# Performance work log

Hardware: AMD Instinct MI355X
Metric: run time of the kernel (lower is better)

## Reference

```python
import jax, jax.numpy as jnp
import numpy as np

D_STATE = 16
DT_RANK = 48
D_CONV = 4
EPS = 1e-5


def rmsnorm(x, w):
    return x * jax.lax.rsqrt(jnp.mean(x * x, axis=-1, keepdims=True) + EPS) * w


def causal_dw_conv(u, w, b):
    # u: [B,T,D], w: [D,K] depthwise causal kernel, b: [D]
    B, T, D = u.shape
    K = w.shape[1]
    up = jnp.pad(u, ((0, 0), (K - 1, 0), (0, 0)))
    acc = jnp.zeros_like(u)
    for k in range(K):  # K=4, tiny fixed loop
        acc = acc + up[:, k:k + T, :] * w[:, k]
    return acc + b


def mamba_mixer(h, ipw, cw, cb, xpw, dpw, dpb, alog, dpar, opw):
    # h: [B,T,d_model]
    B, T, _ = h.shape
    xz = h @ ipw.T                       # [B,T,2*d_inner]
    u, z = jnp.split(xz, 2, axis=-1)     # each [B,T,d_inner]
    u = jax.nn.silu(causal_dw_conv(u, cw, cb))
    xp = u @ xpw.T                       # [B,T,dt_rank+2*d_state]
    dt = xp[..., :DT_RANK]
    Bm = xp[..., DT_RANK:DT_RANK + D_STATE]
    Cm = xp[..., DT_RANK + D_STATE:]
    delta = jax.nn.softplus(dt @ dpw.T + dpb)      # [B,T,d_inner]
    A = -jnp.exp(alog)                              # [d_inner, d_state], negative
    dA = jnp.exp(delta[..., None] * A)              # [B,T,d_inner,d_state] in (0,1)
    dBu = (delta * u)[..., None] * Bm[:, :, None, :]
    # time-major for scan
    dA_t = jnp.moveaxis(dA, 1, 0)
    dBu_t = jnp.moveaxis(dBu, 1, 0)
    C_t = jnp.moveaxis(Cm, 1, 0)

    def step(hst, inp):
        a, bu, c = inp
        hst = a * hst + bu                          # [B,d_inner,d_state]
        y = jnp.einsum('bdn,bn->bd', hst, c)
        return hst, y

    h0 = jnp.zeros((B, u.shape[-1], D_STATE), u.dtype)
    _, ys = jax.lax.scan(step, h0, (dA_t, dBu_t, C_t))
    y = jnp.moveaxis(ys, 0, 1) + u * dpar           # skip via D
    y = y * jax.nn.silu(z)                          # gate
    return y @ opw.T                                # [B,T,d_model]


def setup_inputs() -> dict:
    key = jax.random.key(0)
    ks = jax.random.split(key, 16)
    L, d_model, d_inner = 4, 768, 1536
    B, C, T = 4, 256, 512
    s = 0.02
    return {
        'x': jax.random.normal(ks[0], (B, C, T), jnp.float32),
        'in_proj_w': jax.random.normal(ks[1], (L, 2 * d_inner, d_model), jnp.float32) * s,
        'conv_w': jax.random.normal(ks[2], (L, d_inner, D_CONV), jnp.float32) * 0.3,
        'conv_b': jnp.zeros((L, d_inner), jnp.float32),
        'x_proj_w': jax.random.normal(ks[3], (L, DT_RANK + 2 * D_STATE, d_inner), jnp.float32) * s,
        'dt_proj_w': jax.random.normal(ks[4], (L, d_inner, DT_RANK), jnp.float32) * 0.1,
        'dt_proj_b': jax.random.normal(ks[5], (L, d_inner), jnp.float32) * 0.1 - 4.0,
        'A_log': jax.random.uniform(ks[6], (L, d_inner, D_STATE), jnp.float32, 0.0, 1.5),
        'D_param': jax.random.uniform(ks[7], (L, d_inner), jnp.float32),
        'out_proj_w': jax.random.normal(ks[8], (L, d_model, d_inner), jnp.float32) * s,
        'norm_w': jnp.ones((L, d_model), jnp.float32),
        'norm_f_w': jnp.ones((d_model,), jnp.float32),
        'inp_w': jax.random.normal(ks[9], (d_model, C), jnp.float32) * s,
        'inp_b': jnp.zeros((d_model,), jnp.float32),
        'cls_w': jax.random.normal(ks[10], (10, d_model), jnp.float32) * s,
        'cls_b': jnp.zeros((10,), jnp.float32),
    }


def reference(x, in_proj_w, conv_w, conv_b, x_proj_w, dt_proj_w, dt_proj_b,
              A_log, D_param, out_proj_w, norm_w, norm_f_w,
              inp_w, inp_b, cls_w, cls_b):
    # x: (B, C, T) -> (B, T, C)
    xt = jnp.transpose(x, (0, 2, 1))
    h = xt @ inp_w.T + inp_b                # [B,T,d_model]
    hidden = h
    residual = None
    L = in_proj_w.shape[0]
    for l in range(L):
        residual = hidden if residual is None else hidden + residual
        normed = rmsnorm(residual, norm_w[l])
        hidden = mamba_mixer(normed, in_proj_w[l], conv_w[l], conv_b[l],
                             x_proj_w[l], dt_proj_w[l], dt_proj_b[l],
                             A_log[l], D_param[l], out_proj_w[l])
    residual = hidden + residual
    hidden = rmsnorm(residual, norm_f_w)
    pooled = hidden.mean(axis=1)            # [B,d_model]
    logits = pooled @ cls_w.T + cls_b       # [B,num_labels]
    return logits
```

## Files before the change

### kernel.cpp

```cpp
#include <hip/hip_runtime.h>
#include <math.h>

#define D_MODEL 768
#define D_INNER 1536
#define B_SZ 4
#define T_SZ 512
#define ROWS (B_SZ*T_SZ)
#define XP_N 80
#define CH 16
#define CT 32
#define XS 8
#define XKC (D_INNER/XS)
#define OS 4
#define OKC (D_INNER/OS)
#define MN_OUT (ROWS*768)

typedef __attribute__((ext_vector_type(8))) short bf16x8;
typedef __attribute__((ext_vector_type(4))) float f32x4;

#define GLL(g, l) __builtin_amdgcn_global_load_lds( \
    (const __attribute__((address_space(1))) void*)(g), \
    (__attribute__((address_space(3))) void*)(l), 16, 0, 0)

__device__ __forceinline__ float sigmoidf_(float x){ return 1.0f/(1.0f+__expf(-x)); }
__device__ __forceinline__ float siluf_(float x){ return x*sigmoidf_(x); }
__device__ __forceinline__ unsigned short f2bf(float f){
  unsigned u = __builtin_bit_cast(unsigned, f);
  u = (u + 0x7FFFu + ((u >> 16) & 1u)) >> 16;
  return (unsigned short)u;
}

__global__ __launch_bounds__(256) void gemm_bf16(
    const unsigned short* __restrict__ A, const unsigned short* __restrict__ Wb,
    float* __restrict__ C, int M, int N, int K)
{
  __shared__ unsigned short As[128*32];
  __shared__ unsigned short Ws[128*32];
  const int tid = threadIdx.x;
  const int bm = blockIdx.y*128, bn = blockIdx.x*128;
  const int wave = tid >> 6, lane = tid & 63;
  const int wm = (wave >> 1)*64, wn = (wave & 1)*64;
  const int fr = lane & 15, quad = lane >> 4;
  f32x4 acc[4][4] = {};
  const int row0 = (wave*64 + lane) >> 2;
  const int khp  = lane & 3;
  const int khl  = (khp + 4 - ((row0 >> 1) & 3)) & 3;
  const unsigned short* Ag = A  + (size_t)(bm + row0)*K + khl*8;
  const unsigned short* Wg = Wb + (size_t)(bn + row0)*K + khl*8;
  const size_t rstep = (size_t)64*K;
  unsigned short* ldsA = As + wave*512;
  unsigned short* ldsW = Ws + wave*512;

  for (int k0 = 0; k0 < K; k0 += 32){
    GLL(Ag + k0,          ldsA);
    GLL(Ag + rstep + k0,  ldsA + 2048);
    GLL(Wg + k0,          ldsW);
    GLL(Wg + rstep + k0,  ldsW + 2048);
    __syncthreads();
    bf16x8 a[4], b[4];
    #pragma unroll
    for (int i=0;i<4;i++){
      const int row = wm + i*16 + fr;
      a[i] = *(const bf16x8*)(As + row*32 + (((quad + (row>>1)) & 3)*8));
    }
    #pragma unroll
    for (int j=0;j<4;j++){
      const int row = wn + j*16 + fr;
      b[j] = *(const bf16x8*)(Ws + row*32 + (((quad + (row>>1)) & 3)*8));
    }
    #pragma unroll
    for (int i=0;i<4;i++)
      #pragma unroll
      for (int j=0;j<4;j++)
        acc[i][j] = __builtin_amdgcn_mfma_f32_16x16x32_bf16(a[i], b[j], acc[i][j], 0, 0, 0);
    __syncthreads();
  }
  #pragma unroll
  for (int i=0;i<4;i++){
    #pragma unroll
    for (int r=0;r<4;r++){
      const int row = bm + wm + i*16 + quad*4 + r;
      float* Cp = C + (size_t)row*N + bn + wn + fr;
      #pragma unroll
      for (int j=0;j<4;j++)
        Cp[j*16] = acc[i][j][r];
    }
  }
}

__global__ __launch_bounds__(256) void gemm_bf16_sk(
    const unsigned short* __restrict__ A, const unsigned short* __restrict__ Wb,
    float* __restrict__ P0, float* __restrict__ P1, int M, int N, int K)
{
  __shared__ unsigned short As[128*32];
  __shared__ unsigned short Ws[128*32];
  const int tid = threadIdx.x;
  const int bm = blockIdx.y*128, bn = blockIdx.x*128;
  const int s = blockIdx.z;
  const int koff = s*OKC;
  const int wave = tid >> 6, lane = tid & 63;
  const int wm = (wave >> 1)*64, wn = (wave & 1)*64;
  const int fr = lane & 15, quad = lane >> 4;
  f32x4 acc[4][4] = {};
  const int row0 = (wave*64 + lane) >> 2;
  const int khp  = lane & 3;
  const int khl  = (khp + 4 - ((row0 >> 1) & 3)) & 3;
  const unsigned short* Ag = A  + (size_t)(bm + row0)*K + koff + khl*8;
  const unsigned short* Wg = Wb + (size_t)(bn + row0)*K + koff + khl*8;
  const size_t rstep = (size_t)64*K;
  unsigned short* ldsA = As + wave*512;
  unsigned short* ldsW = Ws + wave*512;

  for (int k0 = 0; k0 < OKC; k0 += 32){
    GLL(Ag + k0,          ldsA);
    GLL(Ag + rstep + k0,  ldsA + 2048);
    GLL(Wg + k0,          ldsW);
    GLL(Wg + rstep + k0,  ldsW + 2048);
    __syncthreads();
    bf16x8 a[4], b[4];
    #pragma unroll
    for (int i=0;i<4;i++){
      const int row = wm + i*16 + fr;
      a[i] = *(const bf16x8*)(As + row*32 + (((quad + (row>>1)) & 3)*8));
    }
    #pragma unroll
    for (int j=0;j<4;j++){
      const int row = wn + j*16 + fr;
      b[j] = *(const bf16x8*)(Ws + row*32 + (((quad + (row>>1)) & 3)*8));
    }
    #pragma unroll
    for (int i=0;i<4;i++)
      #pragma unroll
      for (int j=0;j<4;j++)
        acc[i][j] = __builtin_amdgcn_mfma_f32_16x16x32_bf16(a[i], b[j], acc[i][j], 0, 0, 0);
    __syncthreads();
  }
  float* Cb = (s < 2 ? P0 : P1) + (size_t)(s & 1)*MN_OUT;
  #pragma unroll
  for (int i=0;i<4;i++){
    #pragma unroll
    for (int r=0;r<4;r++){
      const int row = bm + wm + i*16 + quad*4 + r;
      float* Cp = Cb + (size_t)row*N + bn + wn + fr;
      #pragma unroll
      for (int j=0;j<4;j++)
        Cp[j*16] = acc[i][j][r];
    }
  }
}

__global__ __launch_bounds__(256) void sgemm_input(
    const float* __restrict__ x, const float* __restrict__ W,
    const float* __restrict__ bias, float* __restrict__ C)
{
  __shared__ float As[16][64];
  __shared__ float Wsh[16][64];
  const int bm = blockIdx.y*64, bn = blockIdx.x*64;
  const int b = bm >> 9, t0 = bm & (T_SZ-1);
  const int tid = threadIdx.x;
  const int tx = tid & 15, ty = tid >> 4;
  const int lm = tid & 63, lk = (tid >> 6) << 2;
  float acc[4][4] = {};
  const float* Wp = W + (size_t)(bn+lm)*256 + lk;
  const float* xb = x + ((size_t)b*256)*512 + t0 + lm;
  for (int k0 = 0; k0 < 256; k0 += 16){
    #pragma unroll
    for (int i=0;i<4;i++)
      As[lk+i][lm] = xb[(size_t)(k0+lk+i)*512];
    float4 wv = *(const float4*)(Wp + k0);
    Wsh[lk+0][lm]=wv.x; Wsh[lk+1][lm]=wv.y; Wsh[lk+2][lm]=wv.z; Wsh[lk+3][lm]=wv.w;
    __syncthreads();
    #pragma unroll
    for (int k = 0; k < 16; k++){
      float a[4], w[4];
      #pragma unroll
      for (int i=0;i<4;i++) a[i] = As[k][ty*4+i];
      #pragma unroll
      for (int j=0;j<4;j++) w[j] = Wsh[k][tx*4+j];
      #pragma unroll
      for (int i=0;i<4;i++)
        #pragma unroll
        for (int j=0;j<4;j++)
          acc[i][j] += a[i]*w[j];
    }
    __syncthreads();
  }
  #pragma unroll
  for (int i=0;i<4;i++){
    const int r = bm + ty*4 + i;
    #pragma unroll
    for (int j=0;j<4;j++){
      const int n = bn + tx*4 + j;
      C[(size_t)r*768 + n] = acc[i][j] + bias[n];
    }
  }
}

__global__ __launch_bounds__(256) void xproj_conv_splitk(
    const float* __restrict__ xz, const float* __restrict__ cw,
    const float* __restrict__ cb, const float* __restrict__ W,
    float* __restrict__ part)
{
  __shared__ float As[16][64];
  __shared__ float Wsh[16][80];
  const int bm = blockIdx.x*64;
  const int s = blockIdx.y;
  const int koff = s*XKC;
  const int tid = threadIdx.x;
  const int tx = tid & 15, ty = tid >> 4;
  const int lm = tid & 63, lk = (tid >> 6) << 2;
  float acc[4][5] = {};
  const int row = bm + lm;
  const int t = row & (T_SZ-1);
  for (int k0 = 0; k0 < XKC; k0 += 16){
    const int d0 = koff + k0 + lk;
    float4 cbv = *(const float4*)(cb + d0);
    float cba[4] = {cbv.x, cbv.y, cbv.z, cbv.w};
    float4 tp3 = *(const float4*)(xz + (size_t)row*3072 + d0);
    float4 tp0 = (t>=3) ? *(const float4*)(xz + (size_t)(row-3)*3072 + d0) : make_float4(0.f,0.f,0.f,0.f);
    float4 tp1 = (t>=2) ? *(const float4*)(xz + (size_t)(row-2)*3072 + d0) : make_float4(0.f,0.f,0.f,0.f);
    float4 tp2 = (t>=1) ? *(const float4*)(xz + (size_t)(row-1)*3072 + d0) : make_float4(0.f,0.f,0.f,0.f);
    float a0[4]={tp0.x,tp0.y,tp0.z,tp0.w}, a1[4]={tp1.x,tp1.y,tp1.z,tp1.w};
    float a2[4]={tp2.x,tp2.y,tp2.z,tp2.w}, a3[4]={tp3.x,tp3.y,tp3.z,tp3.w};
    #pragma unroll
    for (int i=0;i<4;i++){
      const float4 w4 = *(const float4*)(cw + (size_t)(d0+i)*4);
      float a = cba[i];
      a += a0[i]*w4.x; a += a1[i]*w4.y; a += a2[i]*w4.z; a += a3[i]*w4.w;
      As[lk+i][lm] = siluf_(a);
    }
    for (int i = tid; i < 320; i += 256){
      const int wr = i % 80, wk = (i / 80) << 2;
      float4 wv = *(const float4*)(W + (size_t)wr*D_INNER + koff + k0 + wk);
      Wsh[wk+0][wr]=wv.x; Wsh[wk+1][wr]=wv.y; Wsh[wk+2][wr]=wv.z; Wsh[wk+3][wr]=wv.w;
    }
    __syncthreads();
    #pragma unroll
    for (int k = 0; k < 16; k++){
      float a[4], w[5];
      #pragma unroll
      for (int i=0;i<4;i++) a[i] = As[k][ty*4+i];
      #pragma unroll
      for (int j=0;j<5;j++) w[j] = Wsh[k][tx*5+j];
      #pragma unroll
      for (int i=0;i<4;i++)
        #pragma unroll
        for (int j=0;j<5;j++)
          acc[i][j] += a[i]*w[j];
    }
    __syncthreads();
  }
  #pragma unroll
  for (int i=0;i<4;i++){
    const int r = bm + ty*4 + i;
    #pragma unroll
    for (int j=0;j<5;j++){
      const int n = tx*5 + j;
      part[((size_t)s*ROWS + r)*XP_N + n] = acc[i][j];
    }
  }
}

__global__ __launch_bounds__(256) void dtproj_fused(
    const float* __restrict__ part, const float* __restrict__ W,
    const float* __restrict__ bias, float* __restrict__ delta,
    float* __restrict__ xpbc)
{
  if (blockIdx.x >= 24){
    const int i = ((blockIdx.x - 24)*32 + blockIdx.y)*256 + threadIdx.x;
    const int r = i >> 5, cc = i & 31;
    float ssum = 0.f;
    #pragma unroll
    for (int s2=0;s2<XS;s2++)
      ssum += part[((size_t)s2*ROWS + r)*XP_N + 48 + cc];
    xpbc[(size_t)r*32 + cc] = ssum;
    return;
  }
  __shared__ float As[16][64];
  __shared__ float Wsh[16][64];
  const int bm = blockIdx.y*64, bn = blockIdx.x*64;
  const int tid = threadIdx.x;
  const int tx = tid & 15, ty = tid >> 4;
  const int lm = tid & 63, lk = (tid >> 6) << 2;
  float acc[4][4] = {};
  const float* Ap = part + (size_t)(bm+lm)*XP_N + lk;
  const float* Wp = W + (size_t)(bn+lm)*48 + lk;
  for (int k0 = 0; k0 < 48; k0 += 16){
    float4 av = make_float4(0.f,0.f,0.f,0.f);
    #pragma unroll
    for (int s2=0;s2<XS;s2++){
      const float4 pv = *(const float4*)(Ap + (size_t)s2*ROWS*XP_N + k0);
      av.x += pv.x; av.y += pv.y; av.z += pv.z; av.w += pv.w;
    }
    float4 wv = *(const float4*)(Wp + k0);
    As[lk+0][lm]=av.x; As[lk+1][lm]=av.y; As[lk+2][lm]=av.z; As[lk+3][lm]=av.w;
    Wsh[lk+0][lm]=wv.x; Wsh[lk+1][lm]=wv.y; Wsh[lk+2][lm]=wv.z; Wsh[lk+3][lm]=wv.w;
    __syncthreads();
    #pragma unroll
    for (int k = 0; k < 16; k++){
      float a[4], w[4];
      #pragma unroll
      for (int i=0;i<4;i++) a[i] = As[k][ty*4+i];
      #pragma unroll
      for (int j=0;j<4;j++) w[j] = Wsh[k][tx*4+j];
      #pragma unroll
      for (int i=0;i<4;i++)
        #pragma unroll
        for (int j=0;j<4;j++)
          acc[i][j] += a[i]*w[j];
    }
    __syncthreads();
  }
  #pragma unroll
  for (int i=0;i<4;i++){
    const int r = bm + ty*4 + i;
    #pragma unroll
    for (int j=0;j<4;j++){
      const int n = bn + tx*4 + j;
      float v = acc[i][j] + bias[n];
      v = (v > 20.f) ? v : log1pf(__expf(v));
      delta[(size_t)r*D_INNER + n] = v;
    }
  }
}

__global__ __launch_bounds__(256) void scan_pass1(
    const float* __restrict__ delta, const float* __restrict__ xz,
    const float* __restrict__ xpbc, const float* __restrict__ alog,
    const float* __restrict__ cw, const float* __restrict__ cb,
    float* __restrict__ Pend, float* __restrict__ Hend)
{
  const int d = blockIdx.x*256 + threadIdx.x;
  const int b = blockIdx.y, c = blockIdx.z;
  float4 t0 = *(const float4*)(alog + d*16 + 0);
  float4 t1 = *(const float4*)(alog + d*16 + 4);
  float4 t2 = *(const float4*)(alog + d*16 + 8);
  float4 t3 = *(const float4*)(alog + d*16 + 12);
  float Av[16] = {t0.x,t0.y,t0.z,t0.w,t1.x,t1.y,t1.z,t1.w,
                  t2.x,t2.y,t2.z,t2.w,t3.x,t3.y,t3.z,t3.w};
  float h[16], P[16];
  #pragma unroll
  for (int n=0;n<16;n++){ Av[n] = -__expf(Av[n]); h[n]=0.f; P[n]=1.f; }
  const size_t row0 = (size_t)b*T_SZ + (size_t)c*CT;
  const float* dp  = delta + row0*D_INNER + d;
  const float* xp0 = xz    + row0*3072 + d;
  const float* bp  = xpbc  + row0*32;
  const float4 cwv = *(const float4*)(cw + (size_t)d*4);
  const float cbv = cb[d];
  float xm3, xm2, xm1;
  if (c == 0){ xm3 = xm2 = xm1 = 0.f; }
  else { xm3 = xp0[-3*3072]; xm2 = xp0[-2*3072]; xm1 = xp0[-1*3072]; }
  #pragma unroll 4
  for (int tt=0; tt<CT; tt++){
    const float dv = dp[(size_t)tt*D_INNER];
    const float xc = xp0[(size_t)tt*3072];
    float ua = cbv;
    ua += xm3*cwv.x; ua += xm2*cwv.y; ua += xm1*cwv.z; ua += xc*cwv.w;
    const float uv = siluf_(ua);
    xm3 = xm2; xm2 = xm1; xm1 = xc;
    const float4 B0 = *(const float4*)(bp + (size_t)tt*32);
    const float4 B1 = *(const float4*)(bp + (size_t)tt*32 + 4);
    const float4 B2 = *(const float4*)(bp + (size_t)tt*32 + 8);
    const float4 B3 = *(const float4*)(bp + (size_t)tt*32 + 12);
    const float Bv[16] = {B0.x,B0.y,B0.z,B0.w,B1.x,B1.y,B1.z,B1.w,
                          B2.x,B2.y,B2.z,B2.w,B3.x,B3.y,B3.z,B3.w};
    const float du = dv*uv;
    #pragma unroll
    for (int n=0;n<16;n++){
      const float dA = __expf(dv*Av[n]);
      P[n] *= dA;
      h[n] = dA*h[n] + du*Bv[n];
    }
  }
  float* Pp = Pend + ((size_t)(b*CH+c)*D_INNER + d)*16;
  float* Hp = Hend + ((size_t)(b*CH+c)*D_INNER + d)*16;
  *(float4*)(Pp+ 0) = make_float4(P[0],P[1],P[2],P[3]);
  *(float4*)(Pp+ 4) = make_float4(P[4],P[5],P[6],P[7]);
  *(float4*)(Pp+ 8) = make_float4(P[8],P[9],P[10],P[11]);
  *(float4*)(Pp+12) = make_float4(P[12],P[13],P[14],P[15]);
  *(float4*)(Hp+ 0) = make_float4(h[0],h[1],h[2],h[3]);
  *(float4*)(Hp+ 4) = make_float4(h[4],h[5],h[6],h[7]);
  *(float4*)(Hp+ 8) = make_float4(h[8],h[9],h[10],h[11]);
  *(float4*)(Hp+12) = make_float4(h[12],h[13],h[14],h[15]);
}

__global__ __launch_bounds__(256) void scan_combine(
    const float* __restrict__ Pend, const float* __restrict__ Hend,
    float* __restrict__ Hin)
{
  const int gid = blockIdx.x*256 + threadIdx.x;
  const int b = gid / (D_INNER*16);
  const int r = gid % (D_INNER*16);
  const size_t base = (size_t)b*CH*D_INNER*16 + r;
  const size_t step = (size_t)D_INNER*16;
  float h = 0.f;
  Hin[base] = 0.f;
  #pragma unroll
  for (int c=0; c<CH-1; c++){
    h = Pend[base + (size_t)c*step]*h + Hend[base + (size_t)c*step];
    Hin[base + (size_t)(c+1)*step] = h;
  }
}

__global__ __launch_bounds__(256) void scan_pass3(
    const float* __restrict__ delta, const float* __restrict__ xz,
    const float* __restrict__ xpbc, const float* __restrict__ alog,
    const float* __restrict__ cw, const float* __restrict__ cb,
    const float* __restrict__ Dp, const float* __restrict__ Hin,
    unsigned short* __restrict__ yb)
{
  const int d = blockIdx.x*256 + threadIdx.x;
  const int b = blockIdx.y, c = blockIdx.z;
  float4 t0 = *(const float4*)(alog + d*16 + 0);
  float4 t1 = *(const float4*)(alog + d*16 + 4);
  float4 t2 = *(const float4*)(alog + d*16 + 8);
  float4 t3 = *(const float4*)(alog + d*16 + 12);
  float Av[16] = {t0.x,t0.y,t0.z,t0.w,t1.x,t1.y,t1.z,t1.w,
                  t2.x,t2.y,t2.z,t2.w,t3.x,t3.y,t3.z,t3.w};
  #pragma unroll
  for (int n=0;n<16;n++) Av[n] = -__expf(Av[n]);
  const float* Hp = Hin + ((size_t)(b*CH+c)*D_INNER + d)*16;
  float4 h0 = *(const float4*)(Hp+0);
  float4 h1 = *(const float4*)(Hp+4);
  float4 h2 = *(const float4*)(Hp+8);
  float4 h3 = *(const float4*)(Hp+12);
  float h[16] = {h0.x,h0.y,h0.z,h0.w,h1.x,h1.y,h1.z,h1.w,
                 h2.x,h2.y,h2.z,h2.w,h3.x,h3.y,h3.z,h3.w};
  const float Dv = Dp[d];
  const size_t row0 = (size_t)b*T_SZ + (size_t)c*CT;
  const float* dp  = delta + row0*D_INNER + d;
  const float* xp0 = xz    + row0*3072 + d;
  const float* zp  = xz    + row0*3072 + 1536 + d;
  const float* bp  = xpbc  + row0*32;
  unsigned short* yp = yb + row0*D_INNER + d;
  const float4 cwv = *(const float4*)(cw + (size_t)d*4);
  const float cbv = cb[d];
  float xm3, xm2, xm1;
  if (c == 0){ xm3 = xm2 = xm1 = 0.f; }
  else { xm3 = xp0[-3*3072]; xm2 = xp0[-2*3072]; xm1 = xp0[-1*3072]; }
  #pragma unroll 2
  for (int tt=0; tt<CT; tt++){
    const float dv = dp[(size_t)tt*D_INNER];
    const float xc = xp0[(size_t)tt*3072];
    const float zv = zp[(size_t)tt*3072];
    float ua = cbv;
    ua += xm3*cwv.x; ua += xm2*cwv.y; ua += xm1*cwv.z; ua += xc*cwv.w;
    const float uv = siluf_(ua);
    xm3 = xm2; xm2 = xm1; xm1 = xc;
    const float4 B0 = *(const float4*)(bp + (size_t)tt*32);
    const float4 B1 = *(const float4*)(bp + (size_t)tt*32 + 4);
    const float4 B2 = *(const float4*)(bp + (size_t)tt*32 + 8);
    const float4 B3 = *(const float4*)(bp + (size_t)tt*32 + 12);
    const float4 C0 = *(const float4*)(bp + (size_t)tt*32 + 16);
    const float4 C1 = *(const float4*)(bp + (size_t)tt*32 + 20);
    const float4 C2 = *(const float4*)(bp + (size_t)tt*32 + 24);
    const float4 C3 = *(const float4*)(bp + (size_t)tt*32 + 28);
    const float Bv[16] = {B0.x,B0.y,B0.z,B0.w,B1.x,B1.y,B1.z,B1.w,
                          B2.x,B2.y,B2.z,B2.w,B3.x,B3.y,B3.z,B3.w};
    const float Cv[16] = {C0.x,C0.y,C0.z,C0.w,C1.x,C1.y,C1.z,C1.w,
                          C2.x,C2.y,C2.z,C2.w,C3.x,C3.y,C3.z,C3.w};
    const float du = dv*uv;
    float p = 0.f;
    #pragma unroll
    for (int n=0;n<16;n++){
      const float dA = __expf(dv*Av[n]);
      h[n] = dA*h[n] + du*Bv[n];
      p += h[n]*Cv[n];
    }
    yp[(size_t)tt*D_INNER] = f2bf((p + uv*Dv)*siluf_(zv));
  }
}

__global__ __launch_bounds__(256) void fused_norm_cast(
    float* __restrict__ resid, const float* __restrict__ P0, const float* __restrict__ P1,
    const float* __restrict__ w, unsigned short* __restrict__ obf, float* __restrict__ ofp,
    const float* __restrict__ cin1, unsigned short* __restrict__ co1, int cn1, int cnb1,
    const float* __restrict__ cin2, unsigned short* __restrict__ co2, int cn2)
{
  const int blk = blockIdx.x;
  if (blk >= 2048){
    const int cb = blk - 2048;
    const float* in; unsigned short* o; int i4;
    if (cb < cnb1){ in = cin1; o = co1; i4 = (cb*256 + threadIdx.x)*4; if (i4 >= cn1) return; }
    else { in = cin2; o = co2; i4 = ((cb-cnb1)*256 + threadIdx.x)*4; if (i4 >= cn2) return; }
    float4 v = *(const float4*)(in + i4);
    ushort4 r;
    r.x = f2bf(v.x); r.y = f2bf(v.y); r.z = f2bf(v.z); r.w = f2bf(v.w);
    *(ushort4*)(o + i4) = r;
    return;
  }
  const int row = blk;
  const int tid = threadIdx.x;
  float v[3];
  float ss = 0.f;
  #pragma unroll
  for (int i=0;i<3;i++){
    const int c = tid + i*256;
    const size_t idx = (size_t)row*768 + c;
    float r = resid[idx];
    if (P0) r += (P0[idx] + P0[MN_OUT + idx]) + (P1[idx] + P1[MN_OUT + idx]);
    v[i] = r;
    ss += r*r;
  }
  #pragma unroll
  for (int off=32; off>=1; off>>=1) ss += __shfl_xor(ss, off);
  __shared__ float sred[4];
  const int lane = tid & 63, wv = tid >> 6;
  if (lane == 0) sred[wv] = ss;
  __syncthreads();
  const float tot = sred[0]+sred[1]+sred[2]+sred[3];
  const float scale = rsqrtf(tot*(1.0f/768.0f) + 1e-5f);
  #pragma unroll
  for (int i=0;i<3;i++){
    const int c = tid + i*256;
    const size_t idx = (size_t)row*768 + c;
    if (P0) resid[idx] = v[i];
    const float o = v[i]*scale*w[c];
    if (obf) obf[idx] = f2bf(o);
    else     ofp[idx] = o;
  }
}

__global__ __launch_bounds__(256) void pool_partial(const float* __restrict__ normed,
                                                    float* __restrict__ part){
  const int i = blockIdx.x*256 + threadIdx.x;
  const int s = blockIdx.y;
  const int b = i / 768, m = i % 768;
  float sum = 0.f;
  const float* p = normed + ((size_t)b*T_SZ + s*32)*768 + m;
  #pragma unroll
  for (int t=0; t<32; t++) sum += p[(size_t)t*768];
  part[s*3072 + i] = sum;
}

__global__ __launch_bounds__(256) void pool_cls(const float* __restrict__ part,
                                                const float* __restrict__ cw,
                                                const float* __restrict__ cb,
                                                float* __restrict__ out){
  __shared__ float ls[768];
  const int b = blockIdx.x;
  const int tid = threadIdx.x;
  #pragma unroll
  for (int i=0;i<3;i++){
    const int m = tid + i*256;
    float s = 0.f;
    #pragma unroll
    for (int c=0;c<16;c++) s += part[c*3072 + b*768 + m];
    ls[m] = s * (1.0f/T_SZ);
  }
  __syncthreads();
  const int wave = tid >> 6, lane = tid & 63;
  for (int o = wave; o < 10; o += 4){
    float s = 0.f;
    for (int k = lane; k < 768; k += 64) s += ls[k]*cw[o*768 + k];
    #pragma unroll
    for (int off=32; off>=1; off>>=1) s += __shfl_xor(s, off);
    if (lane == 0) out[b*10 + o] = s + cb[o];
  }
}

extern "C" void kernel_launch(void* const* d_in, const int* in_sizes, int n_in,
                              void* d_out, int out_size, void* d_ws, size_t ws_size,
                              hipStream_t stream) {
  const float* x         = (const float*)d_in[0];
  const float* in_proj_w = (const float*)d_in[1];
  const float* conv_w    = (const float*)d_in[2];
  const float* conv_b    = (const float*)d_in[3];
  const float* x_proj_w  = (const float*)d_in[4];
  const float* dt_proj_w = (const float*)d_in[5];
  const float* dt_proj_b = (const float*)d_in[6];
  const float* A_log     = (const float*)d_in[7];
  const float* D_param   = (const float*)d_in[8];
  const float* out_proj_w= (const float*)d_in[9];
  const float* norm_w    = (const float*)d_in[10];
  const float* norm_f_w  = (const float*)d_in[11];
  const float* inp_w     = (const float*)d_in[12];
  const float* inp_b     = (const float*)d_in[13];
  const float* cls_w     = (const float*)d_in[14];
  const float* cls_b     = (const float*)d_in[15];
  float* out = (float*)d_out;

  char* ws = (char*)d_ws;
  auto carve = [&](size_t nelem)->float* {
    float* p = (float*)ws;
    ws += ((nelem*sizeof(float) + 255)/256)*256;
    return p;
  };
  float* resid  = carve((size_t)ROWS*768);
  float* normed = carve((size_t)ROWS*768);
  float* hidden = carve((size_t)ROWS*768);
  float* xz     = carve((size_t)ROWS*3072);
  float* ucv    = carve((size_t)ROWS*1536);
  float* xpbc   = carve((size_t)ROWS*32);
  float* delta  = carve((size_t)ROWS*1536);
  float* ybf_f  = carve((size_t)ROWS*1536/2);
  float* wbi_f  = carve((size_t)(3072*768)/2);
  float* wbo_f  = carve((size_t)(768*1536)/2);
  float* Hin    = carve((size_t)B_SZ*CH*D_INNER*16);
  float* xpart  = carve((size_t)XS*ROWS*XP_N);
  float* ppool  = carve((size_t)16*3072);

  unsigned short* normedb = (unsigned short*)normed;
  unsigned short* ybf = (unsigned short*)ybf_f;
  unsigned short* wbi = (unsigned short*)wbi_f;
  unsigned short* wbo = (unsigned short*)wbo_f;
  float* Pend = normed;
  float* Hend = hidden;

  sgemm_input<<<dim3(12,32), 256, 0, stream>>>(x, inp_w, inp_b, resid);

  for (int l = 0; l < 4; l++){
    fused_norm_cast<<<2048 + 2304 + 1152, 256, 0, stream>>>(
        resid, l ? delta : nullptr, l ? ucv : nullptr,
        norm_w + (size_t)l*768, normedb, nullptr,
        in_proj_w + (size_t)l*3072*768, wbi, 3072*768, 2304,
        out_proj_w + (size_t)l*768*1536, wbo, 768*1536);
    gemm_bf16<<<dim3(24,16), 256, 0, stream>>>(normedb, wbi, xz, ROWS, 3072, 768);
    xproj_conv_splitk<<<dim3(32,XS), 256, 0, stream>>>(
        xz, conv_w + (size_t)l*1536*4, conv_b + (size_t)l*1536,
        x_proj_w + (size_t)l*XP_N*1536, xpart);
    dtproj_fused<<<dim3(32,32), 256, 0, stream>>>(
        xpart, dt_proj_w + (size_t)l*1536*48, dt_proj_b + (size_t)l*1536, delta, xpbc);
    scan_pass1<<<dim3(6,B_SZ,CH-1), 256, 0, stream>>>(
        delta, xz, xpbc, A_log + (size_t)l*1536*16,
        conv_w + (size_t)l*1536*4, conv_b + (size_t)l*1536, Pend, Hend);
    scan_combine<<<(B_SZ*D_INNER*16)/256, 256, 0, stream>>>(Pend, Hend, Hin);
    scan_pass3<<<dim3(6,B_SZ,CH), 256, 0, stream>>>(
        delta, xz, xpbc, A_log + (size_t)l*1536*16,
        conv_w + (size_t)l*1536*4, conv_b + (size_t)l*1536,
        D_param + (size_t)l*1536, Hin, ybf);
    gemm_bf16_sk<<<dim3(6,16,OS), 256, 0, stream>>>(ybf, wbo, delta, ucv, ROWS, 768, 1536);
  }

  fused_norm_cast<<<2048, 256, 0, stream>>>(
      resid, delta, ucv, norm_f_w, nullptr, normed,
      nullptr, nullptr, 0, 0, nullptr, nullptr, 0);
  pool_partial<<<dim3(12,16), 256, 0, stream>>>(normed, ppool);
  pool_cls<<<4, 256, 0, stream>>>(ppool, cls_w, cls_b, out);
}
```

Baseline: 842.8 us.

## Shrink GEMM M-tile to 64, double scan chunks, compute chunk decay via delta sum

Both bf16 GEMMs now use 64x128 tiles, with each wave owning a 64x32 slab, which doubles the grid to get more blocks onto the CUs. The selective scan moves from 16 chunks of 32 steps to 32 chunks of 16 steps for more parallelism. The per-chunk decay product is now taken as exp(A*sum(delta)) rather than a running product, dropping a multiply per state per step. Pend and Hend get their own workspace buffers because the larger chunk count no longer fits in the aliased normed/hidden buffers; the trade-off is lower MFMA reuse per block and more combine work.

```diff
diff --git a/kernel.cpp b/kernel.cpp
--- a/kernel.cpp
+++ b/kernel.cpp
@@ -7,8 +7,8 @@
 #define T_SZ 512
 #define ROWS (B_SZ*T_SZ)
 #define XP_N 80
-#define CH 16
-#define CT 32
+#define CH 32
+#define CT 16
 #define XS 8
 #define XKC (D_INNER/XS)
 #define OS 4
@@ -34,16 +34,17 @@
     const unsigned short* __restrict__ A, const unsigned short* __restrict__ Wb,
     float* __restrict__ C, int M, int N, int K)
 {
-  __shared__ unsigned short As[128*32];
+  __shared__ unsigned short As[64*32];
   __shared__ unsigned short Ws[128*32];
   const int tid = threadIdx.x;
-  const int bm = blockIdx.y*128, bn = blockIdx.x*128;
+  const int bm = blockIdx.y*64, bn = blockIdx.x*128;
   const int wave = tid >> 6, lane = tid & 63;
-  const int wm = (wave >> 1)*64, wn = (wave & 1)*64;
+  const int wn = wave*32;
   const int fr = lane & 15, quad = lane >> 4;
-  f32x4 acc[4][4] = {};
-  const int row0 = (wave*64 + lane) >> 2;
-  const int khp  = lane & 3;
+  f32x4 acc[4][2] = {};
+  const int chunk = wave*64 + lane;
+  const int row0 = chunk >> 2;
+  const int khp  = chunk & 3;
   const int khl  = (khp + 4 - ((row0 >> 1) & 3)) & 3;
   const unsigned short* Ag = A  + (size_t)(bm + row0)*K + khl*8;
   const unsigned short* Wg = Wb + (size_t)(bn + row0)*K + khl*8;
@@ -53,25 +54,24 @@
 
   for (int k0 = 0; k0 < K; k0 += 32){
     GLL(Ag + k0,          ldsA);
-    GLL(Ag + rstep + k0,  ldsA + 2048);
     GLL(Wg + k0,          ldsW);
     GLL(Wg + rstep + k0,  ldsW + 2048);
     __syncthreads();
-    bf16x8 a[4], b[4];
+    bf16x8 a[4], b[2];
     #pragma unroll
     for (int i=0;i<4;i++){
-      const int row = wm + i*16 + fr;
+      const int row = i*16 + fr;
       a[i] = *(const bf16x8*)(As + row*32 + (((quad + (row>>1)) & 3)*8));
     }
     #pragma unroll
-    for (int j=0;j<4;j++){
+    for (int j=0;j<2;j++){
       const int row = wn + j*16 + fr;
       b[j] = *(const bf16x8*)(Ws + row*32 + (((quad + (row>>1)) & 3)*8));
     }
     #pragma unroll
     for (int i=0;i<4;i++)
       #pragma unroll
-      for (int j=0;j<4;j++)
+      for (int j=0;j<2;j++)
         acc[i][j] = __builtin_amdgcn_mfma_f32_16x16x32_bf16(a[i], b[j], acc[i][j], 0, 0, 0);
     __syncthreads();
   }
@@ -79,10 +79,10 @@
   for (int i=0;i<4;i++){
     #pragma unroll
     for (int r=0;r<4;r++){
-      const int row = bm + wm + i*16 + quad*4 + r;
+      const int row = bm + i*16 + quad*4 + r;
       float* Cp = C + (size_t)row*N + bn + wn + fr;
       #pragma unroll
-      for (int j=0;j<4;j++)
+      for (int j=0;j<2;j++)
         Cp[j*16] = acc[i][j][r];
     }
   }
@@ -92,18 +92,19 @@
     const unsigned short* __restrict__ A, const unsigned short* __restrict__ Wb,
     float* __restrict__ P0, float* __restrict__ P1, int M, int N, int K)
 {
-  __shared__ unsigned short As[128*32];
+  __shared__ unsigned short As[64*32];
   __shared__ unsigned short Ws[128*32];
   const int tid = threadIdx.x;
-  const int bm = blockIdx.y*128, bn = blockIdx.x*128;
+  const int bm = blockIdx.y*64, bn = blockIdx.x*128;
   const int s = blockIdx.z;
   const int koff = s*OKC;
   const int wave = tid >> 6, lane = tid & 63;
-  const int wm = (wave >> 1)*64, wn = (wave & 1)*64;
+  const int wn = wave*32;
   const int fr = lane & 15, quad = lane >> 4;
-  f32x4 acc[4][4] = {};
-  const int row0 = (wave*64 + lane) >> 2;
-  const int khp  = lane & 3;
+  f32x4 acc[4][2] = {};
+  const int chunk = wave*64 + lane;
+  const int row0 = chunk >> 2;
+  const int khp  = chunk & 3;
   const int khl  = (khp + 4 - ((row0 >> 1) & 3)) & 3;
   const unsigned short* Ag = A  + (size_t)(bm + row0)*K + koff + khl*8;
   const unsigned short* Wg = Wb + (size_t)(bn + row0)*K + koff + khl*8;
@@ -113,25 +114,24 @@
 
   for (int k0 = 0; k0 < OKC; k0 += 32){
     GLL(Ag + k0,          ldsA);
-    GLL(Ag + rstep + k0,  ldsA + 2048);
     GLL(Wg + k0,          ldsW);
     GLL(Wg + rstep + k0,  ldsW + 2048);
     __syncthreads();
-    bf16x8 a[4], b[4];
+    bf16x8 a[4], b[2];
     #pragma unroll
     for (int i=0;i<4;i++){
-      const int row = wm + i*16 + fr;
+      const int row = i*16 + fr;
       a[i] = *(const bf16x8*)(As + row*32 + (((quad + (row>>1)) & 3)*8));
     }
     #pragma unroll
-    for (int j=0;j<4;j++){
+    for (int j=0;j<2;j++){
       const int row = wn + j*16 + fr;
       b[j] = *(const bf16x8*)(Ws + row*32 + (((quad + (row>>1)) & 3)*8));
     }
     #pragma unroll
     for (int i=0;i<4;i++)
       #pragma unroll
-      for (int j=0;j<4;j++)
+      for (int j=0;j<2;j++)
         acc[i][j] = __builtin_amdgcn_mfma_f32_16x16x32_bf16(a[i], b[j], acc[i][j], 0, 0, 0);
     __syncthreads();
   }
@@ -140,10 +140,10 @@
   for (int i=0;i<4;i++){
     #pragma unroll
     for (int r=0;r<4;r++){
-      const int row = bm + wm + i*16 + quad*4 + r;
+      const int row = bm + i*16 + quad*4 + r;
       float* Cp = Cb + (size_t)row*N + bn + wn + fr;
       #pragma unroll
-      for (int j=0;j<4;j++)
+      for (int j=0;j<2;j++)
         Cp[j*16] = acc[i][j][r];
     }
   }
@@ -338,9 +338,10 @@
   float4 t3 = *(const float4*)(alog + d*16 + 12);
   float Av[16] = {t0.x,t0.y,t0.z,t0.w,t1.x,t1.y,t1.z,t1.w,
                   t2.x,t2.y,t2.z,t2.w,t3.x,t3.y,t3.z,t3.w};
-  float h[16], P[16];
-  #pragma unroll
-  for (int n=0;n<16;n++){ Av[n] = -__expf(Av[n]); h[n]=0.f; P[n]=1.f; }
+  float h[16];
+  #pragma unroll
+  for (int n=0;n<16;n++){ Av[n] = -__expf(Av[n]); h[n]=0.f; }
+  float sdv = 0.f;
   const size_t row0 = (size_t)b*T_SZ + (size_t)c*CT;
   const float* dp  = delta + row0*D_INNER + d;
   const float* xp0 = xz    + row0*3072 + d;
@@ -365,13 +366,16 @@
     const float Bv[16] = {B0.x,B0.y,B0.z,B0.w,B1.x,B1.y,B1.z,B1.w,
                           B2.x,B2.y,B2.z,B2.w,B3.x,B3.y,B3.z,B3.w};
     const float du = dv*uv;
+    sdv += dv;
     #pragma unroll
     for (int n=0;n<16;n++){
       const float dA = __expf(dv*Av[n]);
-      P[n] *= dA;
       h[n] = dA*h[n] + du*Bv[n];
     }
   }
+  float P[16];
+  #pragma unroll
+  for (int n=0;n<16;n++) P[n] = __expf(Av[n]*sdv);
   float* Pp = Pend + ((size_t)(b*CH+c)*D_INNER + d)*16;
   float* Hp = Hend + ((size_t)(b*CH+c)*D_INNER + d)*16;
   *(float4*)(Pp+ 0) = make_float4(P[0],P[1],P[2],P[3]);
@@ -588,7 +592,6 @@
   };
   float* resid  = carve((size_t)ROWS*768);
   float* normed = carve((size_t)ROWS*768);
-  float* hidden = carve((size_t)ROWS*768);
   float* xz     = carve((size_t)ROWS*3072);
   float* ucv    = carve((size_t)ROWS*1536);
   float* xpbc   = carve((size_t)ROWS*32);
@@ -596,6 +599,8 @@
   float* ybf_f  = carve((size_t)ROWS*1536/2);
   float* wbi_f  = carve((size_t)(3072*768)/2);
   float* wbo_f  = carve((size_t)(768*1536)/2);
+  float* Pend   = carve((size_t)B_SZ*CH*D_INNER*16);
+  float* Hend   = carve((size_t)B_SZ*CH*D_INNER*16);
   float* Hin    = carve((size_t)B_SZ*CH*D_INNER*16);
   float* xpart  = carve((size_t)XS*ROWS*XP_N);
   float* ppool  = carve((size_t)16*3072);
@@ -604,8 +609,6 @@
   unsigned short* ybf = (unsigned short*)ybf_f;
   unsigned short* wbi = (unsigned short*)wbi_f;
   unsigned short* wbo = (unsigned short*)wbo_f;
-  float* Pend = normed;
-  float* Hend = hidden;
 
   sgemm_input<<<dim3(12,32), 256, 0, stream>>>(x, inp_w, inp_b, resid);
 
@@ -615,7 +618,7 @@
         norm_w + (size_t)l*768, normedb, nullptr,
         in_proj_w + (size_t)l*3072*768, wbi, 3072*768, 2304,
         out_proj_w + (size_t)l*768*1536, wbo, 768*1536);
-    gemm_bf16<<<dim3(24,16), 256, 0, stream>>>(normedb, wbi, xz, ROWS, 3072, 768);
+    gemm_bf16<<<dim3(24,32), 256, 0, stream>>>(normedb, wbi, xz, ROWS, 3072, 768);
     xproj_conv_splitk<<<dim3(32,XS), 256, 0, stream>>>(
         xz, conv_w + (size_t)l*1536*4, conv_b + (size_t)l*1536,
         x_proj_w + (size_t)l*XP_N*1536, xpart);
@@ -629,7 +632,7 @@
         delta, xz, xpbc, A_log + (size_t)l*1536*16,
         conv_w + (size_t)l*1536*4, conv_b + (size_t)l*1536,
         D_param + (size_t)l*1536, Hin, ybf);
-    gemm_bf16_sk<<<dim3(6,16,OS), 256, 0, stream>>>(ybf, wbo, delta, ucv, ROWS, 768, 1536);
+    gemm_bf16_sk<<<dim3(6,32,OS), 256, 0, stream>>>(ybf, wbo, delta, ucv, ROWS, 768, 1536);
   }
 
   fused_norm_cast<<<2048, 256, 0, stream>>>(
```

After: 818.5 us. -2.9%, faster.
